# Performance work log

Hardware: AMD Instinct MI355X
Metric: run time of the kernel (lower is better)

Reference implementation:

```python
import jax, jax.numpy as jnp
import numpy as np

# ---- static configuration (matches init_kwargs) ----
N_QUBITS = 11
N_LAYERS = 2
N_HIDDEN = N_QUBITS // 2            # 5
N_VISIBLE = N_QUBITS - N_HIDDEN     # 6
N_PARAMS = N_LAYERS * (3 * N_HIDDEN + (N_HIDDEN - 1) + 3 * N_VISIBLE)  # 74
TWO_PI = 2.0 * np.pi

# Pauli building blocks (numpy constants, complex64)
I2 = np.eye(2, dtype=np.complex64)
X2 = np.array([[0, 1], [1, 0]], dtype=np.complex64)
K2 = np.array([[0, -1], [1, 0]], dtype=np.complex64)   # -i*Y
Z2 = np.array([[1, 0], [0, -1]], dtype=np.complex64)

# PauliZ sign table: wire 0 is the most-significant bit of the flattened state
_idx = np.arange(2 ** N_QUBITS)
SIGNS = np.stack([1.0 - 2.0 * ((_idx >> (N_QUBITS - 1 - q)) & 1)
                  for q in range(N_QUBITS)], 0).astype(np.float32)  # [n_qubits, 2^n]


def _rx(t):
    t = jnp.asarray(t, jnp.float32)
    c, s = jnp.cos(t / 2), jnp.sin(t / 2)
    return (c[..., None, None] * I2 - 1j * s[..., None, None] * X2).astype(jnp.complex64)


def _ry(t):
    t = jnp.asarray(t, jnp.float32)
    c, s = jnp.cos(t / 2), jnp.sin(t / 2)
    return (c[..., None, None] * I2 + s[..., None, None] * K2).astype(jnp.complex64)


def _rz(t):
    t = jnp.asarray(t, jnp.float32)
    c, s = jnp.cos(t / 2), jnp.sin(t / 2)
    return (c[..., None, None] * I2 - 1j * s[..., None, None] * Z2).astype(jnp.complex64)


def _apply_1q(state, gate, q):
    # state: (B,) + (2,)*N_QUBITS ; gate: [2,2] shared or [B,2,2] batched
    s = jnp.moveaxis(state, 1 + q, -1)
    if gate.ndim == 3:
        s = jnp.einsum('bij,b...j->b...i', gate, s)
    else:
        s = jnp.einsum('ij,...j->...i', gate, s)
    return jnp.moveaxis(s, -1, 1 + q)


def _apply_crx(state, theta, c, t):
    # controlled-RX(theta) with control wire c, target wire t (theta scalar)
    sc = jnp.moveaxis(state, [1 + c, 1 + t], [1, 2])
    g = _rx(theta)  # [2,2]
    s1 = jnp.einsum('ij,bj...->bi...', g, sc[:, 1])
    sc = jnp.stack([sc[:, 0], s1], axis=1)
    return jnp.moveaxis(sc, [1, 2], [1 + c, 1 + t])


def _embed_state(angles):
    # Angle embedding: RX(angle_q)|0> on each wire -> product state
    B = angles.shape[0]
    amp = _rx(angles)[..., :, 0]          # [B, n_qubits, 2] (first column = action on |0>)
    st = amp[:, 0]                        # [B, 2]
    for q in range(1, N_QUBITS):
        st = (st[:, :, None] * amp[:, q][:, None, :]).reshape(B, -1)
    return st.reshape((B,) + (2,) * N_QUBITS)


def _circuit(angles, params):
    st = _embed_state(angles)
    p = 0
    for _ in range(N_LAYERS):
        for i in range(N_HIDDEN):
            st = _apply_1q(st, _rx(params[p]), i)
            st = _apply_1q(st, _ry(params[p + 1]), i)
            st = _apply_1q(st, _rz(params[p + 2]), i)
            p += 3
        for i in range(N_HIDDEN - 1):
            st = _apply_crx(st, params[p], i, i + 1)
            p += 1
        for i in range(N_VISIBLE):
            w = N_HIDDEN + i
            st = _apply_1q(st, _rx(params[p]), w)
            st = _apply_1q(st, _ry(params[p + 1]), w)
            st = _apply_1q(st, _rz(params[p + 2]), w)
            p += 3
    probs = (st.real ** 2 + st.imag ** 2).reshape(st.shape[0], -1)  # [B, 2^n]
    return jnp.einsum('bi,qi->bq', probs, SIGNS)  # <Z_q> per qubit, [B, n_qubits]


def _preprocess(x_t):
    # mean-pool feature vector down to n_visible, then min-max scale to [0, 2pi]
    F = x_t.shape[-1]
    step = F // N_VISIBLE
    starts = np.arange(N_VISIBLE) * step
    win = x_t[:, starts[:, None] + np.arange(step)]   # [B, n_visible, step]
    pooled = win.mean(-1)
    mn = pooled.min(-1, keepdims=True)
    mx = pooled.max(-1, keepdims=True)
    return TWO_PI * (pooled - mn) / (mx - mn + 1e-8)


def setup_inputs() -> dict:
    key = jax.random.key(0)
    k1, k2 = jax.random.split(key)
    x = jax.random.normal(k1, (128, 48, 60), dtype=jnp.float32)
    hidden = jnp.zeros((128, N_HIDDEN), dtype=jnp.float32)
    params = jax.random.uniform(k2, (N_PARAMS,), dtype=jnp.float32,
                                minval=0.0, maxval=TWO_PI)
    return {"x": x, "hidden": hidden, "params": params}


def reference(x, hidden, params):
    def body(h, x_t):
        inp = _preprocess(x_t)                         # [B, n_visible]
        angles = jnp.concatenate([h, inp], axis=-1)    # [B, n_qubits]
        z = _circuit(angles, params)                   # [B, n_qubits]
        return z[:, :N_HIDDEN], z[:, N_HIDDEN:]

    xs = jnp.swapaxes(x, 0, 1)                         # [S, B, F]
    hidden_final, outs = jax.lax.scan(body, hidden, xs)
    outputs = jnp.swapaxes(outs, 0, 1)                 # [B, S, n_visible]
    return outputs, hidden_final
```

## Files before the change

### kernel.cpp

```cpp
#include <hip/hip_runtime.h>
#include <math.h>

#define TSTEPS 48
#define FEAT 60
#define BATCH 128
#define BLOCK 256
#define TWO_PI_F 6.2831853071795864769f


struct Cf { float r, i; };
__device__ __forceinline__ Cf cmul(Cf a, Cf b){ return {a.r*b.r - a.i*b.i, a.r*b.i + a.i*b.r}; }
__device__ __forceinline__ Cf cadd(Cf a, Cf b){ return {a.r+b.r, a.i+b.i}; }
__device__ __forceinline__ void mm2(const Cf A[4], const Cf B[4], Cf D[4]) {
  D[0] = cadd(cmul(A[0],B[0]), cmul(A[1],B[2]));
  D[1] = cadd(cmul(A[0],B[1]), cmul(A[1],B[3]));
  D[2] = cadd(cmul(A[2],B[0]), cmul(A[3],B[2]));
  D[3] = cadd(cmul(A[2],B[1]), cmul(A[3],B[3]));
}

__device__ __forceinline__ void fusedU(const float* p, Cf U[4]) {
  float cx = cosf(0.5f*p[0]), sxn = sinf(0.5f*p[0]);
  float cy = cosf(0.5f*p[1]), syn = sinf(0.5f*p[1]);
  float cz = cosf(0.5f*p[2]), szn = sinf(0.5f*p[2]);
  Cf RX[4] = {{cx,0.f},{0.f,-sxn},{0.f,-sxn},{cx,0.f}};
  Cf RY[4] = {{cy,0.f},{-syn,0.f},{syn,0.f},{cy,0.f}};
  Cf RZ[4] = {{cz,-szn},{0.f,0.f},{0.f,0.f},{cz,szn}};
  Cf M[4];
  mm2(RY, RX, M);
  mm2(RZ, M, U);
}

template<int CTRL>
__device__ __forceinline__ float dppf(float v) {
  return __int_as_float(__builtin_amdgcn_mov_dpp(__float_as_int(v), CTRL, 0xF, 0xF, true));
}

template<int M>
__device__ __forceinline__ float sx(float v) {
  if constexpr (M == 1)      return dppf<0xB1>(v);
  else if constexpr (M == 2) return dppf<0x4E>(v);
  else if constexpr (M == 3) return dppf<0x1B>(v);
  else if constexpr (M == 4) return dppf<0x141>(dppf<0x1B>(v));
  else                       return dppf<0x128>(v);
}

template<int M>
__device__ __forceinline__ Cf sxc(Cf v){ return { sx<M>(v.r), sx<M>(v.i) }; }

__device__ __forceinline__ float wave_sum(float v) {
  v += sx<1>(v);
  v += sx<2>(v);
  v += sx<4>(v);
  v += sx<8>(v);
  v += dppf<0x142>(v);
  v += dppf<0x143>(v);
  return __int_as_float(__builtin_amdgcn_readlane(__float_as_int(v), 63));
}

__device__ __forceinline__ float2 conjmul(float2 a, float2 b) {
  return make_float2(a.x*b.x + a.y*b.y, a.x*b.y - a.y*b.x);
}

template<int M>
__device__ __forceinline__ void lane_u(Cf A[4], const Cf U[4], int hi) {
  Cf ca = hi ? U[3] : U[0];
  Cf cb = hi ? U[2] : U[1];
  #pragma unroll
  for (int r = 0; r < 4; ++r) {
    Cf o = sxc<M>(A[r]);
    A[r] = cadd(cmul(ca, A[r]), cmul(cb, o));
  }
}
template<int M>
__device__ __forceinline__ void lane_crx(Cf A[4], float c, float s, int cv) {
  float cc = cv ? c : 1.f, ss = cv ? s : 0.f;
  #pragma unroll
  for (int r = 0; r < 4; ++r) {
    Cf o = sxc<M>(A[r]);
    A[r] = { cc*A[r].r + ss*o.i, cc*A[r].i - ss*o.r };
  }
}
__device__ __forceinline__ void reg_u_b1(Cf A[4], const Cf U[4]) {
  #pragma unroll
  for (int k = 0; k < 2; ++k) {
    Cf a0 = A[k], a1 = A[k+2];
    A[k]   = cadd(cmul(U[0], a0), cmul(U[1], a1));
    A[k+2] = cadd(cmul(U[2], a0), cmul(U[3], a1));
  }
}
__device__ __forceinline__ void reg_u_b0(Cf A[4], const Cf U[4]) {
  #pragma unroll
  for (int k = 0; k < 4; k += 2) {
    Cf a0 = A[k], a1 = A[k+1];
    A[k]   = cadd(cmul(U[0], a0), cmul(U[1], a1));
    A[k+1] = cadd(cmul(U[2], a0), cmul(U[3], a1));
  }
}
__device__ __forceinline__ void reg_crx_b1(Cf A[4], float c, float s, int cv) {
  float cc = cv ? c : 1.f, ss = cv ? s : 0.f;
  #pragma unroll
  for (int k = 0; k < 2; ++k) {
    Cf a0 = A[k], a1 = A[k+2];
    A[k]   = { cc*a0.r + ss*a1.i, cc*a0.i - ss*a1.r };
    A[k+2] = { ss*a0.i + cc*a1.r, -ss*a0.r + cc*a1.i };
  }
}
__device__ __forceinline__ void reg_crx_b0c1(Cf A[4], float c, float s) {
  Cf a0 = A[2], a1 = A[3];
  A[2] = { c*a0.r + s*a1.i, c*a0.i - s*a1.r };
  A[3] = { s*a0.i + c*a1.r, -s*a0.r + c*a1.i };
}

template<int NTs, int D>
__device__ __forceinline__ void stageK(const float2* __restrict__ src,
                                       float2* __restrict__ dst,
                                       const float2* __restrict__ Pq, int tid) {
  const int total = 5*3*NTs*D*D;
  for (int tau = tid; tau < total; tau += BLOCK) {
    int K = tau % D;
    int J = (tau / D) % D;
    int rest = tau / (D*D);
    int t = rest % NTs;
    int s = (rest / NTs) % 3;
    int m = rest / (3*NTs);
    const float2* Sb = src + (m*NTs + t)*(4*D*D);
    const float2* Pm = Pq + s*4;
    float ax = 0.f, ay = 0.f;
    #pragma unroll
    for (int a = 0; a < 2; ++a)
      #pragma unroll
      for (int bb = 0; bb < 2; ++bb) {
        float2 g = Sb[(2*J+a)*(2*D) + (2*K+bb)];
        float2 p = Pm[bb*2 + a];
        ax += g.x*p.x - g.y*p.y;
        ay += g.x*p.y + g.y*p.x;
      }
    dst[tau] = make_float2(ax, ay);
  }
}

__global__ __launch_bounds__(BLOCK)
void qrnn_kernel(const float* __restrict__ x, const float* __restrict__ hin,
                 const float* __restrict__ params, float* __restrict__ out) {
  __shared__ __align__(16) char bufA[30720];
  __shared__ __align__(16) char bufB[23040];
  __shared__ float coefL[5*256];
  __shared__ float2 Pl[5*12];
  __shared__ float2 U2l[5*4];
  __shared__ float crxcl[8], crxsl[8];
  __shared__ float Wl[6*8];

  const int b   = blockIdx.x;
  const int tid = threadIdx.x;

  float2* Vp  = (float2*)bufB;
  float4* Vp4 = (float4*)bufB;
  float2* A1  = (float2*)bufA;
  float2* A2  = (float2*)bufB;
  float2* A3  = (float2*)bufA;
  float2* A4  = (float2*)bufB;

  if (tid < 5) {
    int q = tid;
    Cf U1[4]; fusedU(params + 3*q, U1);
    Cf T[4] = {U1[0], {-U1[1].r,-U1[1].i}, U1[2], {-U1[3].r,-U1[3].i}};
    Cf Ud[4] = {{U1[0].r,-U1[0].i},{U1[2].r,-U1[2].i},
                {U1[1].r,-U1[1].i},{U1[3].r,-U1[3].i}};
    Cf Zt[4]; mm2(T, Ud, Zt);
    Cf Ty[4] = {{-U1[1].i, U1[1].r}, {U1[0].i, -U1[0].r},
                {-U1[3].i, U1[3].r}, {U1[2].i, -U1[2].r}};
    Cf Yt[4]; mm2(Ty, Ud, Yt);
    float2* P = Pl + q*12;
    P[0] = make_float2(1.f,0.f); P[1] = make_float2(0.f,0.f);
    P[2] = make_float2(0.f,0.f); P[3] = make_float2(1.f,0.f);
    #pragma unroll
    for (int e = 0; e < 4; ++e) P[4+e] = make_float2(Zt[e].r, Zt[e].i);
    #pragma unroll
    for (int e = 0; e < 4; ++e) P[8+e] = make_float2(-Yt[e].r, -Yt[e].i);
  } else if (tid >= 8 && tid < 13) {
    int q = tid - 8;
    Cf U2[4]; fusedU(params + 37 + 3*q, U2);
    #pragma unroll
    for (int e = 0; e < 4; ++e) U2l[q*4+e] = make_float2(U2[e].r, U2[e].i);
  } else if (tid >= 16 && tid < 24) {
    int i = tid - 16;
    float th = (i < 4) ? params[15 + i] : params[52 + (i - 4)];
    crxcl[i] = cosf(0.5f*th); crxsl[i] = sinf(0.5f*th);
  } else if (tid >= 24 && tid < 30) {
    int k = tid - 24;
    Cf Ua[4], Ub[4], W[4];
    fusedU(params + 19 + 3*k, Ua);
    fusedU(params + 56 + 3*k, Ub);
    mm2(Ub, Ua, W);
    #pragma unroll
    for (int e = 0; e < 4; ++e) { Wl[k*8+2*e] = W[e].r; Wl[k*8+2*e+1] = W[e].i; }
  }
  __syncthreads();

  {
    const int quad = tid & 7, col = tid >> 3;
    const int vb2 = quad & 1, vb3 = (quad >> 1) & 1, vb4 = quad >> 2;
    Cf A[4];
    #pragma unroll
    for (int r = 0; r < 4; ++r)
      A[r] = { ((quad<<2)|r) == col ? 1.f : 0.f, 0.f };
    Cf U2g[5][4];
    #pragma unroll
    for (int q = 0; q < 5; ++q)
      #pragma unroll
      for (int e = 0; e < 4; ++e)
        U2g[q][e] = { U2l[q*4+e].x, U2l[q*4+e].y };
    float c_[8], s_[8];
    #pragma unroll
    for (int g = 0; g < 8; ++g) { c_[g] = crxcl[g]; s_[g] = crxsl[g]; }
    lane_crx<2>(A, c_[0], s_[0], vb4);
    lane_crx<1>(A, c_[1], s_[1], vb3);
    reg_crx_b1 (A, c_[2], s_[2], vb2);
    reg_crx_b0c1(A, c_[3], s_[3]);
    lane_u<4>(A, U2g[0], vb4);
    lane_u<2>(A, U2g[1], vb3);
    lane_u<1>(A, U2g[2], vb2);
    reg_u_b1 (A, U2g[3]);
    reg_u_b0 (A, U2g[4]);
    lane_crx<2>(A, c_[4], s_[4], vb4);
    lane_crx<1>(A, c_[5], s_[5], vb3);
    reg_crx_b1 (A, c_[6], s_[6], vb2);
    reg_crx_b0c1(A, c_[7], s_[7]);
    #pragma unroll
    for (int r = 0; r < 4; ++r)
      Vp[((quad<<2)|r)*32 + col] = make_float2(A[r].r, A[r].i);
  }
  __syncthreads();

  {
    const int jt = tid >> 4, kt = tid & 15;
    float2 T[2][2], Bm[5][2][2];
    #pragma unroll
    for (int a = 0; a < 2; ++a)
      #pragma unroll
      for (int c2 = 0; c2 < 2; ++c2) {
        T[a][c2] = make_float2(0.f, 0.f);
        #pragma unroll
        for (int m = 0; m < 5; ++m) Bm[m][a][c2] = make_float2(0.f, 0.f);
      }
    #pragma unroll
    for (int i = 0; i < 32; ++i) {
      float4 vj = Vp4[i*16 + jt], vk = Vp4[i*16 + kt];
      float2 vj0{vj.x,vj.y}, vj1{vj.z,vj.w}, vk0{vk.x,vk.y}, vk1{vk.z,vk.w};
      float2 p[2][2] = {{conjmul(vj0,vk0), conjmul(vj0,vk1)},
                        {conjmul(vj1,vk0), conjmul(vj1,vk1)}};
      #pragma unroll
      for (int a = 0; a < 2; ++a)
        #pragma unroll
        for (int c2 = 0; c2 < 2; ++c2) {
          T[a][c2].x += p[a][c2].x; T[a][c2].y += p[a][c2].y;
        }
      #pragma unroll
      for (int m = 0; m < 5; ++m)
        if (i & (16 >> m)) {
          #pragma unroll
          for (int a = 0; a < 2; ++a)
            #pragma unroll
            for (int c2 = 0; c2 < 2; ++c2) {
              Bm[m][a][c2].x += p[a][c2].x; Bm[m][a][c2].y += p[a][c2].y;
            }
        }
    }
    float2 P4[12];
    #pragma unroll
    for (int e = 0; e < 12; ++e) P4[e] = Pl[4*12 + e];
    #pragma unroll
    for (int m = 0; m < 5; ++m) {
      float2 G[2][2];
      #pragma unroll
      for (int a = 0; a < 2; ++a)
        #pragma unroll
        for (int c2 = 0; c2 < 2; ++c2)
          G[a][c2] = make_float2(T[a][c2].x - 2.f*Bm[m][a][c2].x,
                                 T[a][c2].y - 2.f*Bm[m][a][c2].y);
      #pragma unroll
      for (int s = 0; s < 3; ++s) {
        float ax = 0.f, ay = 0.f;
        #pragma unroll
        for (int a = 0; a < 2; ++a)
          #pragma unroll
          for (int bb = 0; bb < 2; ++bb) {
            float2 g = G[a][bb];
            float2 p = P4[s*4 + bb*2 + a];
            ax += g.x*p.x - g.y*p.y;
            ay += g.x*p.y + g.y*p.x;
          }
        A1[(m*3 + s)*256 + (jt<<4) + kt] = make_float2(ax, ay);
      }
    }
  }
  __syncthreads();

  stageK<3, 8>(A1, A2, Pl + 3*12, tid);  __syncthreads();
  stageK<9, 4>(A2, A3, Pl + 2*12, tid);  __syncthreads();
  stageK<27,2>(A3, A4, Pl + 1*12, tid);  __syncthreads();
  for (int tau = tid; tau < 5*256; tau += BLOCK) {
    int n = tau & 255, m = tau >> 8;
    float val = 0.f;
    if (n < 243) {
      int t = n % 81, s = n / 81;
      const float2* Sb = A4 + (m*81 + t)*4;
      const float2* Pm = Pl + s*4;
      float ax = 0.f;
      #pragma unroll
      for (int a = 0; a < 2; ++a)
        #pragma unroll
        for (int bb = 0; bb < 2; ++bb) {
          float2 g = Sb[a*2 + bb];
          float2 p = Pm[bb*2 + a];
          ax += g.x*p.x - g.y*p.y;
        }
      val = ax * (1.f/32.f);
    }
    coefL[tau] = val;
  }
  __syncthreads();

  const int w = tid >> 6, lane = tid & 63;
  if (w == 0) {
    float sA[4][5], sB[4][5], sC[4][5], cf[5][4];
    #pragma unroll
    for (int j = 0; j < 4; ++j) {
      int n = j*64 + lane;
      int nn = (n < 243) ? n : 0;
      int d0 = nn/81; int rm = nn - d0*81;
      int d1 = rm/27; rm -= d1*27;
      int d2 = rm/9;  rm -= d2*9;
      int d3 = rm/3;  int d4 = rm - d3*3;
      int dq[5] = {d0, d1, d2, d3, d4};
      #pragma unroll
      for (int q = 0; q < 5; ++q) {
        sA[j][q] = (dq[q] == 0) ? 1.f : 0.f;
        sB[j][q] = (dq[q] == 1) ? 1.f : 0.f;
        sC[j][q] = (dq[q] == 2) ? 1.f : 0.f;
      }
      #pragma unroll
      for (int m = 0; m < 5; ++m) cf[m][j] = coefL[m*256 + n];
    }
    const float* hp = hin + b*5;
    float h0 = hp[0], h1 = hp[1], h2 = hp[2], h3 = hp[3], h4 = hp[4];
    #pragma unroll 1
    for (int t = 0; t < TSTEPS; ++t) {
      float cq[5] = {__cosf(h0), __cosf(h1), __cosf(h2), __cosf(h3), __cosf(h4)};
      float sq[5] = {__sinf(h0), __sinf(h1), __sinf(h2), __sinf(h3), __sinf(h4)};
      float mono[4];
      #pragma unroll
      for (int j = 0; j < 4; ++j) {
        float f0 = fmaf(sB[j][0], cq[0], fmaf(sC[j][0], sq[0], sA[j][0]));
        float f1 = fmaf(sB[j][1], cq[1], fmaf(sC[j][1], sq[1], sA[j][1]));
        float f2 = fmaf(sB[j][2], cq[2], fmaf(sC[j][2], sq[2], sA[j][2]));
        float f3 = fmaf(sB[j][3], cq[3], fmaf(sC[j][3], sq[3], sA[j][3]));
        float f4 = fmaf(sB[j][4], cq[4], fmaf(sC[j][4], sq[4], sA[j][4]));
        mono[j] = ((f0*f1)*(f2*f3))*f4;
      }
      float hn[5];
      #pragma unroll
      for (int m = 0; m < 5; ++m) {
        float p01 = fmaf(cf[m][1], mono[1], cf[m][0]*mono[0]);
        float p23 = fmaf(cf[m][3], mono[3], cf[m][2]*mono[2]);
        hn[m] = wave_sum(p01 + p23);
      }
      h0 = hn[0]; h1 = hn[1]; h2 = hn[2]; h3 = hn[3]; h4 = hn[4];
    }
    if (lane < 5) {
      float hv = (lane==0) ? h0 : (lane==1) ? h1 : (lane==2) ? h2
               : (lane==3) ? h3 : h4;
      out[BATCH*TSTEPS*6 + b*5 + lane] = hv;
    }
  } else if (w == 1 && lane < TSTEPS) {
    const float* xp = x + (size_t)b*(TSTEPS*FEAT) + lane*FEAT;
    const float4* xp4 = (const float4*)xp;
    float4 vv[15];
    #pragma unroll
    for (int i2 = 0; i2 < 15; ++i2) vv[i2] = xp4[i2];
    float el[60];
    #pragma unroll
    for (int i2 = 0; i2 < 15; ++i2) {
      el[4*i2+0] = vv[i2].x; el[4*i2+1] = vv[i2].y;
      el[4*i2+2] = vv[i2].z; el[4*i2+3] = vv[i2].w;
    }
    float pooled[6];
    #pragma unroll
    for (int k = 0; k < 6; ++k) {
      float s = 0.f;
      #pragma unroll
      for (int f = 0; f < 10; ++f) s += el[k*10 + f];
      pooled[k] = s * 0.1f;
    }
    float mn = pooled[0], mx = pooled[0];
    #pragma unroll
    for (int v2 = 1; v2 < 6; ++v2) {
      mn = fminf(mn, pooled[v2]); mx = fmaxf(mx, pooled[v2]);
    }
    float* op = out + (size_t)b*(TSTEPS*6) + lane*6;
    #pragma unroll
    for (int k = 0; k < 6; ++k) {
      float W0r = Wl[k*8+0], W0i = Wl[k*8+1], W1r = Wl[k*8+2], W1i = Wl[k*8+3];
      float W2r = Wl[k*8+4], W2i = Wl[k*8+5], W3r = Wl[k*8+6], W3i = Wl[k*8+7];
      float ang = TWO_PI_F * (pooled[k] - mn) / (mx - mn + 1e-8f);
      float ch = __cosf(0.5f*ang), sh = __sinf(0.5f*ang);
      float v0r = W0r*ch + W1i*sh, v0i = W0i*ch - W1r*sh;
      float v1r = W2r*ch + W3i*sh, v1i = W2i*ch - W3r*sh;
      op[k] = (v0r*v0r + v0i*v0i) - (v1r*v1r + v1i*v1i);
    }
  }
}

extern "C" void kernel_launch(void* const* d_in, const int* in_sizes, int n_in,
                              void* d_out, int out_size, void* d_ws, size_t ws_size,
                              hipStream_t stream) {
  const float* x      = (const float*)d_in[0];
  const float* hidden = (const float*)d_in[1];
  const float* params = (const float*)d_in[2];
  float* out          = (float*)d_out;
  qrnn_kernel<<<dim3(BATCH), dim3(BLOCK), 0, stream>>>(x, hidden, params, out);
}
```

Before: 89.17 us.

## Use packed FP32 math, fast trig, and row_shr DPP in serial recurrence

Switches the gate-setup trig from precise cosf/sinf to the fast __cosf/__sinf intrinsics. It also spreads the setup work across different waves instead of keeping it all in wave 0. The serial 48-step hidden-state loop now uses v_pk_fma/v_pk_mul packed FP32 instructions, so each instruction handles two monomial slots and the loop needs fewer instructions. The wave reduction uses row_shr DPP patterns instead of the xor-style swizzles. Fast trig loses accuracy, and the inline asm limits how freely the compiler can schedule.

```diff
diff --git a/kernel.cpp b/kernel.cpp
--- a/kernel.cpp
+++ b/kernel.cpp
@@ -19,9 +19,9 @@
 }
 
 __device__ __forceinline__ void fusedU(const float* p, Cf U[4]) {
-  float cx = cosf(0.5f*p[0]), sxn = sinf(0.5f*p[0]);
-  float cy = cosf(0.5f*p[1]), syn = sinf(0.5f*p[1]);
-  float cz = cosf(0.5f*p[2]), szn = sinf(0.5f*p[2]);
+  float cx = __cosf(0.5f*p[0]), sxn = __sinf(0.5f*p[0]);
+  float cy = __cosf(0.5f*p[1]), syn = __sinf(0.5f*p[1]);
+  float cz = __cosf(0.5f*p[2]), szn = __sinf(0.5f*p[2]);
   Cf RX[4] = {{cx,0.f},{0.f,-sxn},{0.f,-sxn},{cx,0.f}};
   Cf RY[4] = {{cy,0.f},{-syn,0.f},{syn,0.f},{cy,0.f}};
   Cf RZ[4] = {{cz,-szn},{0.f,0.f},{0.f,0.f},{cz,szn}};
@@ -48,13 +48,25 @@
 __device__ __forceinline__ Cf sxc(Cf v){ return { sx<M>(v.r), sx<M>(v.i) }; }
 
 __device__ __forceinline__ float wave_sum(float v) {
-  v += sx<1>(v);
-  v += sx<2>(v);
-  v += sx<4>(v);
-  v += sx<8>(v);
+  v += dppf<0x121>(v);
+  v += dppf<0x122>(v);
+  v += dppf<0x124>(v);
+  v += dppf<0x128>(v);
   v += dppf<0x142>(v);
   v += dppf<0x143>(v);
   return __int_as_float(__builtin_amdgcn_readlane(__float_as_int(v), 63));
+}
+
+typedef float v2f __attribute__((ext_vector_type(2)));
+__device__ __forceinline__ v2f pk_fma(v2f a, v2f b, v2f c) {
+  v2f d;
+  asm("v_pk_fma_f32 %0, %1, %2, %3" : "=v"(d) : "v"(a), "v"(b), "v"(c));
+  return d;
+}
+__device__ __forceinline__ v2f pk_mul(v2f a, v2f b) {
+  v2f d;
+  asm("v_pk_mul_f32 %0, %1, %2" : "=v"(d) : "v"(a), "v"(b));
+  return d;
 }
 
 __device__ __forceinline__ float2 conjmul(float2 a, float2 b) {
@@ -177,17 +189,17 @@
     for (int e = 0; e < 4; ++e) P[4+e] = make_float2(Zt[e].r, Zt[e].i);
     #pragma unroll
     for (int e = 0; e < 4; ++e) P[8+e] = make_float2(-Yt[e].r, -Yt[e].i);
-  } else if (tid >= 8 && tid < 13) {
-    int q = tid - 8;
+  } else if (tid >= 64 && tid < 69) {
+    int q = tid - 64;
     Cf U2[4]; fusedU(params + 37 + 3*q, U2);
     #pragma unroll
     for (int e = 0; e < 4; ++e) U2l[q*4+e] = make_float2(U2[e].r, U2[e].i);
-  } else if (tid >= 16 && tid < 24) {
-    int i = tid - 16;
+  } else if (tid >= 128 && tid < 136) {
+    int i = tid - 128;
     float th = (i < 4) ? params[15 + i] : params[52 + (i - 4)];
-    crxcl[i] = cosf(0.5f*th); crxsl[i] = sinf(0.5f*th);
-  } else if (tid >= 24 && tid < 30) {
-    int k = tid - 24;
+    crxcl[i] = __cosf(0.5f*th); crxsl[i] = __sinf(0.5f*th);
+  } else if (tid >= 192 && tid < 198) {
+    int k = tid - 192;
     Cf Ua[4], Ub[4], W[4];
     fusedU(params + 19 + 3*k, Ua);
     fusedU(params + 56 + 3*k, Ub);
@@ -323,24 +335,38 @@
 
   const int w = tid >> 6, lane = tid & 63;
   if (w == 0) {
-    float sA[4][5], sB[4][5], sC[4][5], cf[5][4];
-    #pragma unroll
-    for (int j = 0; j < 4; ++j) {
-      int n = j*64 + lane;
-      int nn = (n < 243) ? n : 0;
-      int d0 = nn/81; int rm = nn - d0*81;
-      int d1 = rm/27; rm -= d1*27;
-      int d2 = rm/9;  rm -= d2*9;
-      int d3 = rm/3;  int d4 = rm - d3*3;
-      int dq[5] = {d0, d1, d2, d3, d4};
-      #pragma unroll
-      for (int q = 0; q < 5; ++q) {
-        sA[j][q] = (dq[q] == 0) ? 1.f : 0.f;
-        sB[j][q] = (dq[q] == 1) ? 1.f : 0.f;
-        sC[j][q] = (dq[q] == 2) ? 1.f : 0.f;
-      }
-      #pragma unroll
-      for (int m = 0; m < 5; ++m) cf[m][j] = coefL[m*256 + n];
+    v2f sAp[2][5], sBp[2][5], sCp[2][5], cfp[5][2];
+    #pragma unroll
+    for (int s = 0; s < 2; ++s) {
+      #pragma unroll
+      for (int half = 0; half < 2; ++half) {
+        int n = (2*s + half)*64 + lane;
+        int nn = (n < 243) ? n : 0;
+        int d0 = nn/81; int rm = nn - d0*81;
+        int d1 = rm/27; rm -= d1*27;
+        int d2 = rm/9;  rm -= d2*9;
+        int d3 = rm/3;  int d4 = rm - d3*3;
+        int dq[5] = {d0, d1, d2, d3, d4};
+        #pragma unroll
+        for (int q = 0; q < 5; ++q) {
+          if (half == 0) {
+            sAp[s][q].x = (dq[q] == 0) ? 1.f : 0.f;
+            sBp[s][q].x = (dq[q] == 1) ? 1.f : 0.f;
+            sCp[s][q].x = (dq[q] == 2) ? 1.f : 0.f;
+          } else {
+            sAp[s][q].y = (dq[q] == 0) ? 1.f : 0.f;
+            sBp[s][q].y = (dq[q] == 1) ? 1.f : 0.f;
+            sCp[s][q].y = (dq[q] == 2) ? 1.f : 0.f;
+          }
+        }
+      }
+    }
+    #pragma unroll
+    for (int m = 0; m < 5; ++m) {
+      cfp[m][0].x = coefL[m*256 + lane];
+      cfp[m][0].y = coefL[m*256 + lane + 64];
+      cfp[m][1].x = coefL[m*256 + lane + 128];
+      cfp[m][1].y = coefL[m*256 + lane + 192];
     }
     const float* hp = hin + b*5;
     float h0 = hp[0], h1 = hp[1], h2 = hp[2], h3 = hp[3], h4 = hp[4];
@@ -348,22 +374,28 @@
     for (int t = 0; t < TSTEPS; ++t) {
       float cq[5] = {__cosf(h0), __cosf(h1), __cosf(h2), __cosf(h3), __cosf(h4)};
       float sq[5] = {__sinf(h0), __sinf(h1), __sinf(h2), __sinf(h3), __sinf(h4)};
-      float mono[4];
-      #pragma unroll
-      for (int j = 0; j < 4; ++j) {
-        float f0 = fmaf(sB[j][0], cq[0], fmaf(sC[j][0], sq[0], sA[j][0]));
-        float f1 = fmaf(sB[j][1], cq[1], fmaf(sC[j][1], sq[1], sA[j][1]));
-        float f2 = fmaf(sB[j][2], cq[2], fmaf(sC[j][2], sq[2], sA[j][2]));
-        float f3 = fmaf(sB[j][3], cq[3], fmaf(sC[j][3], sq[3], sA[j][3]));
-        float f4 = fmaf(sB[j][4], cq[4], fmaf(sC[j][4], sq[4], sA[j][4]));
-        mono[j] = ((f0*f1)*(f2*f3))*f4;
+      v2f cqp[5], sqp[5];
+      #pragma unroll
+      for (int q = 0; q < 5; ++q) {
+        cqp[q] = (v2f){cq[q], cq[q]};
+        sqp[q] = (v2f){sq[q], sq[q]};
+      }
+      v2f monoP[2];
+      #pragma unroll
+      for (int s = 0; s < 2; ++s) {
+        v2f f0 = pk_fma(sBp[s][0], cqp[0], pk_fma(sCp[s][0], sqp[0], sAp[s][0]));
+        v2f f1 = pk_fma(sBp[s][1], cqp[1], pk_fma(sCp[s][1], sqp[1], sAp[s][1]));
+        v2f f2 = pk_fma(sBp[s][2], cqp[2], pk_fma(sCp[s][2], sqp[2], sAp[s][2]));
+        v2f f3 = pk_fma(sBp[s][3], cqp[3], pk_fma(sCp[s][3], sqp[3], sAp[s][3]));
+        v2f f4 = pk_fma(sBp[s][4], cqp[4], pk_fma(sCp[s][4], sqp[4], sAp[s][4]));
+        monoP[s] = pk_mul(pk_mul(pk_mul(f0, f1), pk_mul(f2, f3)), f4);
       }
       float hn[5];
       #pragma unroll
       for (int m = 0; m < 5; ++m) {
-        float p01 = fmaf(cf[m][1], mono[1], cf[m][0]*mono[0]);
-        float p23 = fmaf(cf[m][3], mono[3], cf[m][2]*mono[2]);
-        hn[m] = wave_sum(p01 + p23);
+        v2f tacc = pk_mul(monoP[0], cfp[m][0]);
+        tacc = pk_fma(monoP[1], cfp[m][1], tacc);
+        hn[m] = wave_sum(tacc.x + tacc.y);
       }
       h0 = hn[0]; h1 = hn[1]; h2 = hn[2]; h3 = hn[3]; h4 = hn[4];
     }
```

After: 83.67 us. 6.2% less time.
